# Kernel optimization log

Hardware: AMD Instinct MI355X
Metric: run time of the kernel (lower is better)

## Reference

```python
import jax, jax.numpy as jnp
import numpy as np
from jax import lax

IMG = 224.0
IOU_THRESH = 0.5

def box_cxcywh_to_xyxy(b):
    cx, cy, w, h = b[..., 0], b[..., 1], b[..., 2], b[..., 3]
    return jnp.stack([cx - 0.5 * w, cy - 0.5 * h, cx + 0.5 * w, cy + 0.5 * h], axis=-1)

def box_iou(a, b):
    area_a = (a[:, 2] - a[:, 0]) * (a[:, 3] - a[:, 1])
    area_b = (b[:, 2] - b[:, 0]) * (b[:, 3] - b[:, 1])
    lt = jnp.maximum(a[:, None, :2], b[None, :, :2])
    rb = jnp.minimum(a[:, None, 2:], b[None, :, 2:])
    wh = jnp.clip(rb - lt, 0.0)
    inter = wh[..., 0] * wh[..., 1]
    return inter / (area_a[:, None] + area_b[None, :] - inter)

def gumbel_softmax(key, logits, axis, tau=1.0):
    # straight-through hard gumbel-softmax (matches torch hard=True)
    g = jax.random.gumbel(key, logits.shape, logits.dtype)
    y = jax.nn.softmax((logits + g) / tau, axis=axis)
    y_hard = jax.nn.one_hot(jnp.argmax(y, axis=axis), y.shape[axis], axis=axis, dtype=y.dtype)
    return y + lax.stop_gradient(y_hard - y)

def nms_indices(boxes, scores, thresh):
    # iterative greedy NMS, returns kept indices in descending-score order (as torchvision)
    n = boxes.shape[0]
    order = jnp.argsort(-scores)
    b = boxes[order]
    areas = (b[:, 2] - b[:, 0]) * (b[:, 3] - b[:, 1])
    pos = jnp.arange(n)
    def body(i, suppressed):
        bi = b[i]
        lt = jnp.maximum(bi[:2], b[:, :2])
        rb = jnp.minimum(bi[2:], b[:, 2:])
        wh = jnp.clip(rb - lt, 0.0)
        inter = wh[:, 0] * wh[:, 1]
        iou = inter / (areas[i] + areas - inter)
        sup = (iou > thresh) & (pos > i) & jnp.logical_not(suppressed[i])
        return suppressed | sup
    suppressed = lax.fori_loop(0, n, body, jnp.zeros((n,), bool))
    keep = np.asarray(jnp.logical_not(suppressed))
    return jnp.asarray(np.asarray(order)[keep])

def _keys():
    return jax.random.split(jax.random.key(42), 3)

def _boxes_and_scores(classencodings, pred_logits, pred_boxes, tgt_ids, batch_idx, tgt_bbox, k0):
    C = classencodings.shape[0]
    B, Q, D = pred_logits.shape
    similarity = jnp.einsum('bqd,cd->bqc', pred_logits, classencodings)
    out_scores = jnp.max(similarity, axis=-1)
    clt = gumbel_softmax(k0, similarity, axis=-1)                      # [B,Q,C] hard
    offx = jnp.arange(C, dtype=pred_logits.dtype) * IMG
    offy = jnp.arange(B, dtype=pred_logits.dtype) * IMG
    ox = jnp.sum(clt * offx, axis=-1)                                  # [B,Q]
    oy = jnp.broadcast_to(offy[:, None], (B, Q))
    out_off = jnp.tile(jnp.stack([ox, oy], axis=-1), (1, 1, 2))        # [B,Q,4]
    out_bbox = (box_cxcywh_to_xyxy(pred_boxes) + out_off).reshape(-1, 4)
    f = pred_logits.dtype
    gt_off = jnp.tile(jnp.stack([IMG * tgt_ids.astype(f), IMG * batch_idx.astype(f)], axis=-1), (1, 2))
    tb = box_cxcywh_to_xyxy(tgt_bbox) + gt_off                         # [N,4]
    return similarity, out_scores.reshape(-1), out_bbox, tb

def ce_diag(logits):
    # CrossEntropyLoss(mean) with targets arange(n)
    return -jnp.mean(jnp.diagonal(jax.nn.log_softmax(logits, axis=1)))

def _forward(classencodings, pred_logits, pred_boxes, pred_masks, tgt_masks, tgt_embs, tgt_bbox, tgt_ids, batch_idx, nms_idx):
    k0, k1, k2 = _keys()
    B, Q, D = pred_logits.shape
    N = tgt_embs.shape[0]
    W, H = tgt_masks.shape[-2:]
    similarity, out_scores, out_bbox, tb = _boxes_and_scores(classencodings, pred_logits, pred_boxes, tgt_ids, batch_idx, tgt_bbox, k0)
    kept = out_bbox[nms_idx]                                           # [K,4]
    K = kept.shape[0]
    iou = box_iou(kept, tb)
    iou = jnp.where(jnp.isnan(iou), 0.0, iou)
    gt_log = jax.nn.softmax(iou, axis=1)
    gt_one_hot = gumbel_softmax(k1, gt_log, axis=1)                    # [K,N]
    gt_sel = gt_one_hot.T @ kept                                       # [N,4]
    gt_ious = jnp.diagonal(box_iou(gt_sel, tb))
    out_embs = gt_one_hot.T @ pred_logits.reshape(-1, D)[nms_idx]      # [N,D]
    class_loss = ce_diag(tgt_embs @ out_embs.T) + ce_diag(out_embs @ tgt_embs.T)
    scores = jnp.einsum('bqd,nd->bqn', pred_logits, tgt_embs).reshape(B * Q, N)
    ind = gumbel_softmax(k2, scores, axis=0).T                         # [N,B*Q]
    om = (ind @ pred_masks.reshape(B * Q, -1)).reshape(N, W, H)
    overall_mask_loss = jnp.mean((om - tgt_masks) ** 2)
    ocm = jnp.einsum('qwh,bcq->bcwh', om, similarity) / om.shape[1]    # [B,Q,W,H] (N==C==Q)
    ocm = jax.nn.softmax(ocm, axis=1)
    batch_lookup = jax.nn.one_hot(batch_idx, B, dtype=pred_logits.dtype).T  # [B,N]
    gt_sim = tgt_embs @ classencodings.T                               # [N,C]
    tsim = batch_lookup[:, :, None] * gt_sim[None, :, :]               # [B,N,C]
    gt_cm = jnp.einsum('bnc,nwh->bcwh', tsim, tgt_masks)               # [B,C,W,H]
    inp = ocm.reshape(B, -1)
    tgt = gt_cm.reshape(B, -1)
    dice = jnp.mean(jnp.sum(inp * tgt) / (jnp.sum(inp, -1) + jnp.sum(tgt, -1) + 1e-6))
    l1 = jnp.abs(gt_sel - tb).sum()
    return jnp.stack([class_loss, dice, overall_mask_loss / K, (1.0 - gt_ious).sum() / K, l1 / K])

def setup_inputs():
    key = jax.random.key(0)
    ks = jax.random.split(key, 10)
    B, Q, C, N, D, W, H = 8, 300, 300, 300, 256, 96, 96
    return {
        'classencodings': jax.random.normal(ks[0], (C, D), jnp.float32),
        'pred_logits': jax.random.normal(ks[1], (B, Q, D), jnp.float32),
        'pred_boxes': jax.random.uniform(ks[2], (B, Q, 4), jnp.float32),
        'pred_masks': jax.random.normal(ks[3], (B * Q, W, H), jnp.float32),
        'tgt_masks': jax.random.uniform(ks[4], (N, W, H), jnp.float32),
        'tgt_embs': jax.random.normal(ks[5], (N, D), jnp.float32),
        'tgt_bbox': jax.random.uniform(ks[6], (N, 4), jnp.float32),
        'im_masks': jnp.ones((B, 224, 224), jnp.float32),
        'tgt_ids': jax.random.randint(ks[7], (N,), 0, C, jnp.int32),
        'batch_idx': jnp.sort(jax.random.randint(ks[8], (N,), 0, B, jnp.int32)),
    }

def reference(classencodings, pred_logits, pred_boxes, pred_masks, tgt_masks, tgt_embs, tgt_bbox, im_masks, tgt_ids, batch_idx):
    k0, _, _ = _keys()
    _, scores, out_bbox, _ = _boxes_and_scores(classencodings, pred_logits, pred_boxes, tgt_ids, batch_idx, tgt_bbox, k0)
    nms_idx = nms_indices(out_bbox, scores, IOU_THRESH)
    return _forward(classencodings, pred_logits, pred_boxes, pred_masks, tgt_masks, tgt_embs, tgt_bbox, tgt_ids, batch_idx, nms_idx)
```

## Files before the change

### kernel.cpp

```cpp
#include <hip/hip_runtime.h>
#include <stdint.h>

#define DEVFN __device__ __forceinline__

typedef unsigned short u16;
typedef short bf16x8 __attribute__((ext_vector_type(8)));
typedef float f32x4 __attribute__((ext_vector_type(4)));

constexpr int BB = 8, QQ = 300, CC = 300, NN = 300, DD = 256;
constexpr int WHX = 9216, BQ = 2400, SIMW = 600;
constexpr int QP = 320;
constexpr int CP = 304;
constexpr int KP = 96;
constexpr int NP = 416;
constexpr int CELLCAP = 300;

constexpr size_t F_SIMS   = 0;
constexpr size_t F_GTSIM  = F_SIMS   + (size_t)BQ*SIMW;
constexpr size_t F_MM     = F_GTSIM  + (size_t)NN*CC;
constexpr size_t F_SCORE  = F_MM     + (size_t)NN*NN;
constexpr size_t F_BBOX   = F_SCORE  + BQ;
constexpr size_t F_TB     = F_BBOX   + (size_t)BQ*4;
constexpr size_t F_SB     = F_TB     + (size_t)NN*4;
constexpr size_t F_SAREA  = F_SB     + (size_t)BQ*4;
constexpr size_t F_KB     = F_SAREA  + BQ;
constexpr size_t F_ROWSUM = F_KB     + (size_t)BQ*4;
constexpr size_t F_OE     = F_ROWSUM + NN;
constexpr size_t F_GSEL   = F_OE     + (size_t)NN*DD;
constexpr size_t F_MSUM   = F_GSEL   + (size_t)NN*4;
constexpr size_t F_STGT   = F_MSUM   + NN;
constexpr size_t F_SC     = F_STGT   + 8;
constexpr size_t F_CNT    = F_SC     + 16;
constexpr size_t F_ACCEND = F_CNT    + BQ;
constexpr size_t F_ORDER  = F_ACCEND;
constexpr size_t F_NMSIDX = F_ORDER  + BQ;
constexpr size_t F_SEL2   = F_NMSIDX + BQ;
constexpr size_t F_BSTART = F_SEL2   + NN;
constexpr size_t F_KINT   = F_BSTART + 16;
constexpr size_t F_CLS    = F_KINT   + 4;
constexpr size_t F_KEEPF  = F_CLS    + BQ;
constexpr size_t F_LIST   = F_KEEPF  + BQ;
constexpr size_t F_S2T    = F_LIST   + (size_t)BQ*CELLCAP;
constexpr size_t F_SIMTB  = ((F_S2T + (size_t)NN*BQ + 7) & ~(size_t)7);
constexpr size_t F_OMT    = F_SIMTB + (size_t)BB*CP*QP/2;
constexpr size_t F_TMT    = F_OMT   + (size_t)WHX*QP/2;
constexpr size_t F_GTP    = F_TMT   + (size_t)WHX*NP/2;
constexpr size_t F_TOTAL  = F_GTP   + (size_t)BB*CP*KP/2;

DEVFN uint32_t rotl32(uint32_t v, int r){ return (v << r) | (v >> (32 - r)); }

DEVFN void tf2x32(uint32_t k0, uint32_t k1, uint32_t x0, uint32_t x1,
                  uint32_t& o0, uint32_t& o1){
  uint32_t ks2 = k0 ^ k1 ^ 0x1BD11BDAu;
  x0 += k0; x1 += k1;
#define TFR(r) x0 += x1; x1 = rotl32(x1, r); x1 ^= x0;
  TFR(13) TFR(15) TFR(26) TFR(6)   x0 += k1;  x1 += ks2 + 1u;
  TFR(17) TFR(29) TFR(16) TFR(24)  x0 += ks2; x1 += k0  + 2u;
  TFR(13) TFR(15) TFR(26) TFR(6)   x0 += k0;  x1 += k1  + 3u;
  TFR(17) TFR(29) TFR(16) TFR(24)  x0 += k1;  x1 += ks2 + 4u;
  TFR(13) TFR(15) TFR(26) TFR(6)   x0 += ks2; x1 += k0  + 5u;
#undef TFR
  o0 = x0; o1 = x1;
}

DEVFN void subkey(int i, uint32_t& k0, uint32_t& k1){
  tf2x32(0u, 42u, 0u, (uint32_t)i, k0, k1);
}

DEVFN float gumbel32(uint32_t k0, uint32_t k1, uint32_t idx){
  uint32_t h, l; tf2x32(k0, k1, 0u, idx, h, l);
  uint32_t bits = h ^ l;
  float f = __uint_as_float((bits >> 9) | 0x3F800000u) - 1.0f;
  const float tiny = 1.17549435e-38f;
  float u = fmaxf(tiny, f + tiny);
  return -logf(-logf(u));
}

DEVFN float iou_xyxy(float ax1,float ay1,float ax2,float ay2,
                     float bx1,float by1,float bx2,float by2){
  float aa = (ax2-ax1)*(ay2-ay1);
  float ab = (bx2-bx1)*(by2-by1);
  float lx = fmaxf(ax1,bx1), ly = fmaxf(ay1,by1);
  float rx = fminf(ax2,bx2), ry = fminf(ay2,by2);
  float iw = fmaxf(rx-lx,0.f), ih = fmaxf(ry-ly,0.f);
  float in_ = iw*ih;
  return in_/(aa+ab-in_);
}

DEVFN u16 f2bf(float x){
  uint32_t u = __float_as_uint(x);
  uint32_t r = u + 0x7FFFu + ((u >> 16) & 1u);
  return (u16)(r >> 16);
}

DEVFN void gload_lds16(const u16* g, u16* l){
  __builtin_amdgcn_global_load_lds(
      (const __attribute__((address_space(1))) unsigned int*)g,
      (__attribute__((address_space(3))) unsigned int*)l,
      16, 0, 0);
}

__global__ __launch_bounds__(256) void k_gemm_t(
    const float* __restrict__ pl, const float* __restrict__ ce,
    const float* __restrict__ te, float* __restrict__ sims,
    float* __restrict__ gtsim, float* __restrict__ s2t){
  __shared__ float As[16][64];
  __shared__ float Bs[16][64];
  const int row0 = blockIdx.x * 64, col0 = blockIdx.y * 64;
  const int tid = threadIdx.x;
  const int lrow = tid >> 2, lk0 = (tid & 3) * 4;
  const int tr = tid >> 4, tc = tid & 15;

  float acc[4][4];
  #pragma unroll
  for (int i = 0; i < 4; i++)
    #pragma unroll
    for (int j = 0; j < 4; j++) acc[i][j] = 0.f;

  const float4 z4 = {0.f,0.f,0.f,0.f};
  const int grow = row0 + lrow;
  const int gcol = col0 + lrow;
  const float* arow = nullptr;
  if (grow < 2400) arow = pl + (size_t)grow * DD;
  else if (grow < 2700) arow = te + (size_t)(grow - 2400) * DD;
  const float* brow = nullptr;
  if (gcol < 300) brow = ce + (size_t)gcol * DD;
  else if (gcol < 600) brow = te + (size_t)(gcol - 300) * DD;

  float4 av = arow ? *(const float4*)(arow + lk0) : z4;
  float4 bv = brow ? *(const float4*)(brow + lk0) : z4;

  for (int step = 0; step < 16; step++){
    __syncthreads();
    #pragma unroll
    for (int j = 0; j < 4; j++){
      As[lk0 + j][lrow] = ((const float*)&av)[j];
      Bs[lk0 + j][lrow] = ((const float*)&bv)[j];
    }
    __syncthreads();
    if (step + 1 < 16){
      const int k0 = (step + 1) * 16;
      av = arow ? *(const float4*)(arow + k0 + lk0) : z4;
      bv = brow ? *(const float4*)(brow + k0 + lk0) : z4;
    }
    #pragma unroll
    for (int kk = 0; kk < 16; kk++){
      float4 a4 = *(const float4*)&As[kk][tr*4];
      float4 b4 = *(const float4*)&Bs[kk][tc*4];
      float a[4] = {a4.x,a4.y,a4.z,a4.w};
      float b[4] = {b4.x,b4.y,b4.z,b4.w};
      #pragma unroll
      for (int i = 0; i < 4; i++)
        #pragma unroll
        for (int j = 0; j < 4; j++)
          acc[i][j] = fmaf(a[i], b[j], acc[i][j]);
    }
  }

  #pragma unroll
  for (int i = 0; i < 4; i++){
    const int r = row0 + tr*4 + i;
    const int c0 = col0 + tc*4;
    if (r < 2400){
      if (c0 < 600){
        float4 o0 = {acc[i][0],acc[i][1],acc[i][2],acc[i][3]};
        *(float4*)(sims + (size_t)r*SIMW + c0) = o0;
        if (c0 >= 300){
          #pragma unroll
          for (int j = 0; j < 4; j++)
            s2t[(size_t)(c0 + j - 300)*BQ + r] = acc[i][j];
        }
      }
    } else if (r < 2700){
      const int n = r - 2400;
      #pragma unroll
      for (int j = 0; j < 4; j++){
        int c = c0 + j;
        if (c < 300) gtsim[(size_t)n*CC + c] = acc[i][j];
      }
    }
  }
}

__global__ __launch_bounds__(64) void k_post(
    const float* __restrict__ sims, const float* __restrict__ pb,
    const float* __restrict__ tbb, const int* __restrict__ tids,
    const int* __restrict__ bidx, const float* __restrict__ gtsim,
    float* __restrict__ score, float* __restrict__ bbox,
    float* __restrict__ tb, float* __restrict__ rowsum,
    int* __restrict__ clsout){
  const int bq = blockIdx.x;
  const int lane = threadIdx.x;
  float v[5];
  #pragma unroll
  for (int k = 0; k < 5; k++){
    int c = lane + 64*k;
    v[k] = (c < CC) ? sims[(size_t)bq*SIMW + c] : -INFINITY;
  }
  float mx = v[0];
  #pragma unroll
  for (int k = 1; k < 5; k++) mx = fmaxf(mx, v[k]);
  #pragma unroll
  for (int o = 1; o < 64; o <<= 1) mx = fmaxf(mx, __shfl_xor(mx, o));
  if (lane == 0) score[bq] = mx;

  uint32_t gk0, gk1; subkey(0, gk0, gk1);
  float besty = -INFINITY; int besti = 0x7fffffff;
  #pragma unroll
  for (int k = 0; k < 5; k++){
    int c = lane + 64*k;
    if (c < CC){
      float y = v[k] + gumbel32(gk0, gk1, (uint32_t)(bq*CC + c));
      if (y > besty || (y == besty && c < besti)){ besty = y; besti = c; }
    }
  }
  #pragma unroll
  for (int o = 1; o < 64; o <<= 1){
    float oy = __shfl_xor(besty, o);
    int   oi = __shfl_xor(besti, o);
    if (oy > besty || (oy == besty && oi < besti)){ besty = oy; besti = oi; }
  }
  if (lane == 0){
    int cls = besti;
    clsout[bq] = cls;
    float ox = 224.0f * (float)cls;
    float oy2 = 224.0f * (float)(bq / QQ);
    float cx = pb[bq*4+0], cy = pb[bq*4+1], ww = pb[bq*4+2], hh = pb[bq*4+3];
    bbox[bq*4+0] = cx - 0.5f*ww + ox;
    bbox[bq*4+1] = cy - 0.5f*hh + oy2;
    bbox[bq*4+2] = cx + 0.5f*ww + ox;
    bbox[bq*4+3] = cy + 0.5f*hh + oy2;
  }
  if (bq < NN){
    float rs = 0.f;
    #pragma unroll
    for (int k = 0; k < 5; k++){
      int c = lane + 64*k;
      if (c < CC) rs += gtsim[(size_t)bq*CC + c];
    }
    #pragma unroll
    for (int o = 1; o < 64; o <<= 1) rs += __shfl_xor(rs, o);
    if (lane == 0) rowsum[bq] = rs;
    if (lane == 1){
      float gx = 224.0f * (float)tids[bq], gy = 224.0f * (float)bidx[bq];
      float cx = tbb[bq*4+0], cy = tbb[bq*4+1], ww = tbb[bq*4+2], hh = tbb[bq*4+3];
      tb[bq*4+0] = cx - 0.5f*ww + gx;
      tb[bq*4+1] = cy - 0.5f*hh + gy;
      tb[bq*4+2] = cx + 0.5f*ww + gx;
      tb[bq*4+3] = cy + 0.5f*hh + gy;
    }
  }
}

__global__ __launch_bounds__(256) void k_rankgather(
    const float* __restrict__ score, const float* __restrict__ bbox,
    const int* __restrict__ cls, const int* __restrict__ bidx,
    int* __restrict__ order, float* __restrict__ sb,
    int* __restrict__ bstart, int* __restrict__ cnt,
    int* __restrict__ list){
  const int t = blockIdx.x;
  const int tid = threadIdx.x;
  const float st = score[t];
  int c = 0;
  for (int j = tid; j < BQ; j += 256){
    float sj = score[j];
    c += (sj > st) || (sj == st && j < t);
  }
  #pragma unroll
  for (int o = 1; o < 64; o <<= 1) c += __shfl_xor(c, o);
  __shared__ int wsum[4];
  if ((tid & 63) == 0) wsum[tid >> 6] = c;
  __syncthreads();
  if (tid == 0){
    int r = wsum[0] + wsum[1] + wsum[2] + wsum[3];
    order[r] = t;
    float x1 = bbox[t*4+0], y1 = bbox[t*4+1], x2 = bbox[t*4+2], y2 = bbox[t*4+3];
    sb[r*4+0] = x1; sb[r*4+1] = y1; sb[r*4+2] = x2; sb[r*4+3] = y2;
    int key = (t / QQ) * CC + cls[t];
    int slot = atomicAdd(&cnt[key], 1);
    list[(size_t)key*CELLCAP + slot] = r;
  }
  if (t == 0 && tid >= 32 && tid < 41){
    int b = tid - 32, cb = 0;
    for (int n = 0; n < NN; n++) cb += (bidx[n] < b);
    bstart[b] = cb;
  }
}

__global__ __launch_bounds__(256) void k_cellnms(
    const float* __restrict__ sb, const int* __restrict__ cnt,
    const int* __restrict__ list, int* __restrict__ keepf){
  int key = blockIdx.x*256 + threadIdx.x;
  if (key >= BB*CC) return;
  int m = cnt[key];
  if (m <= 0) return;
  const int* lst = list + (size_t)key*CELLCAP;
  unsigned long long keptmask = 0ull;
  int prevp = -1;
  for (int a = 0; a < m; a++){
    int pa = 0x7fffffff;
    for (int j = 0; j < m; j++){
      int pj = lst[j];
      if (pj > prevp && pj < pa) pa = pj;
    }
    prevp = pa;
    float4 A = ((const float4*)sb)[pa];
    float areaA = (A.z-A.x)*(A.w-A.y);
    bool kept = true;
    int pbprev = -1;
    for (int b2 = 0; b2 < a; b2++){
      int pb = 0x7fffffff;
      for (int j = 0; j < m; j++){
        int pj = lst[j];
        if (pj > pbprev && pj < pb) pb = pj;
      }
      pbprev = pb;
      bool keptb = (m <= 64) ? (((keptmask >> b2) & 1ull) != 0ull) : (keepf[pb] != 0);
      if (!keptb) continue;
      float4 B = ((const float4*)sb)[pb];
      float areaB = (B.z-B.x)*(B.w-B.y);
      float lx = fmaxf(A.x,B.x), ly = fmaxf(A.y,B.y);
      float rx = fminf(A.z,B.z), ry = fminf(A.w,B.w);
      float iw = fmaxf(rx-lx,0.f), ih = fmaxf(ry-ly,0.f);
      float inter = iw*ih;
      if (inter/(areaA + areaB - inter) > 0.5f){ kept = false; break; }
    }
    if (m <= 64 && kept) keptmask |= (1ull << a);
    keepf[pa] = kept ? 1 : 0;
  }
}

__global__ __launch_bounds__(256) void k_compact(
    const int* __restrict__ keepflag, const int* __restrict__ order,
    const float* __restrict__ sb, int* __restrict__ nmsidx,
    float* __restrict__ kb, int* __restrict__ kint){
  __shared__ int csum[256];
  int tid = threadIdx.x;
  int p0 = tid*10;
  int keepf[10];
  int cnt = 0;
  #pragma unroll
  for (int d = 0; d < 10; d++){
    int p = p0 + d;
    int k = 0;
    if (p < BQ) k = keepflag[p];
    keepf[d] = k; cnt += k;
  }
  csum[tid] = cnt; __syncthreads();
  for (int s = 1; s < 256; s <<= 1){
    int add = (tid >= s) ? csum[tid - s] : 0;
    __syncthreads();
    csum[tid] += add;
    __syncthreads();
  }
  int pos = csum[tid] - cnt;
  #pragma unroll
  for (int d = 0; d < 10; d++){
    if (keepf[d]){
      int p = p0 + d;
      nmsidx[pos] = order[p];
      ((float4*)kb)[pos] = ((const float4*)sb)[p];
      pos++;
    }
  }
  if (tid == 255) kint[0] = csum[255];
}

__global__ __launch_bounds__(64) void k_gtsel(
    const float* __restrict__ kb, const float* __restrict__ tb,
    const int* __restrict__ nmsidx, const float* __restrict__ pl,
    const int* __restrict__ kint, float* __restrict__ gsel,
    float* __restrict__ oe){
  const int k = blockIdx.x;
  if (k >= kint[0]) return;
  const int lane = threadIdx.x;
  float4 a = ((const float4*)kb)[k];
  float iou[5];
  float mx = -INFINITY;
  #pragma unroll
  for (int j = 0; j < 5; j++){
    int n = lane + 64*j;
    if (n < NN){
      float4 t = ((const float4*)tb)[n];
      float u = iou_xyxy(a.x,a.y,a.z,a.w, t.x,t.y,t.z,t.w);
      if (u != u) u = 0.f;
      iou[j] = u;
      mx = fmaxf(mx, u);
    } else iou[j] = -INFINITY;
  }
  #pragma unroll
  for (int o = 1; o < 64; o <<= 1) mx = fmaxf(mx, __shfl_xor(mx, o));
  float e[5];
  float ssum = 0.f;
  #pragma unroll
  for (int j = 0; j < 5; j++){
    int n = lane + 64*j;
    e[j] = (n < NN) ? expf(iou[j] - mx) : 0.f;
    ssum += e[j];
  }
  #pragma unroll
  for (int o = 1; o < 64; o <<= 1) ssum += __shfl_xor(ssum, o);
  uint32_t gk0, gk1; subkey(1, gk0, gk1);
  float besty = -INFINITY; int besti = 0x7fffffff;
  #pragma unroll
  for (int j = 0; j < 5; j++){
    int n = lane + 64*j;
    if (n < NN){
      float y = e[j] / ssum + gumbel32(gk0, gk1, (uint32_t)(k*NN + n));
      if (y > besty || (y == besty && n < besti)){ besty = y; besti = n; }
    }
  }
  #pragma unroll
  for (int o = 1; o < 64; o <<= 1){
    float oy = __shfl_xor(besty, o);
    int   oi = __shfl_xor(besti, o);
    if (oy > besty || (oy == besty && oi < besti)){ besty = oy; besti = oi; }
  }
  const int sel = besti;
  if (lane < 4) atomicAdd(&gsel[sel*4 + lane], ((const float*)&a)[lane]);
  const float* plrow = pl + (size_t)nmsidx[k]*DD;
  #pragma unroll
  for (int j = 0; j < 4; j++){
    int c = lane + 64*j;
    atomicAdd(&oe[(size_t)sel*DD + c], plrow[c]);
  }
}

__global__ __launch_bounds__(256) void k_m_t(
    const float* __restrict__ te, const float* __restrict__ oe,
    float* __restrict__ M){
  __shared__ float As[16][32];
  __shared__ float Bs[16][32];
  const int row0 = blockIdx.x * 32, col0 = blockIdx.y * 32;
  const int tid = threadIdx.x;
  const int lr = tid >> 3, lk0 = (tid & 7) * 2;
  const int tr = tid >> 4, tc = tid & 15;
  float acc[2][2] = {{0.f,0.f},{0.f,0.f}};
  const float* arow = (row0 + lr < NN) ? te + (size_t)(row0 + lr)*DD : nullptr;
  const float* brow = (col0 + lr < NN) ? oe + (size_t)(col0 + lr)*DD : nullptr;
  for (int step = 0; step < 16; step++){
    const int k0 = step*16;
    float2 a2 = arow ? *(const float2*)(arow + k0 + lk0) : float2{0.f,0.f};
    float2 b2 = brow ? *(const float2*)(brow + k0 + lk0) : float2{0.f,0.f};
    __syncthreads();
    As[lk0][lr] = a2.x; As[lk0+1][lr] = a2.y;
    Bs[lk0][lr] = b2.x; Bs[lk0+1][lr] = b2.y;
    __syncthreads();
    #pragma unroll
    for (int kk = 0; kk < 16; kk++){
      float a0 = As[kk][tr*2], a1 = As[kk][tr*2+1];
      float b0 = Bs[kk][tc*2], b1 = Bs[kk][tc*2+1];
      acc[0][0] = fmaf(a0,b0,acc[0][0]);
      acc[0][1] = fmaf(a0,b1,acc[0][1]);
      acc[1][0] = fmaf(a1,b0,acc[1][0]);
      acc[1][1] = fmaf(a1,b1,acc[1][1]);
    }
  }
  #pragma unroll
  for (int i = 0; i < 2; i++){
    int r = row0 + tr*2 + i;
    if (r >= NN) continue;
    #pragma unroll
    for (int j = 0; j < 2; j++){
      int c = col0 + tc*2 + j;
      if (c < NN) M[(size_t)r*NN + c] = acc[i][j];
    }
  }
}

__global__ __launch_bounds__(64) void k_ce(
    const float* __restrict__ M, float* __restrict__ sc){
  int i = blockIdx.x, lane = threadIdx.x;
  float m = -INFINITY;
  for (int j = lane; j < NN; j += 64) m = fmaxf(m, M[(size_t)i*NN + j]);
  for (int o = 32; o > 0; o >>= 1) m = fmaxf(m, __shfl_xor(m, o));
  float s = 0.f;
  for (int j = lane; j < NN; j += 64) s += expf(M[(size_t)i*NN + j] - m);
  for (int o = 32; o > 0; o >>= 1) s += __shfl_xor(s, o);
  float lr = m + logf(s);
  float m2 = -INFINITY;
  for (int j = lane; j < NN; j += 64) m2 = fmaxf(m2, M[(size_t)j*NN + i]);
  for (int o = 32; o > 0; o >>= 1) m2 = fmaxf(m2, __shfl_xor(m2, o));
  float s2 = 0.f;
  for (int j = lane; j < NN; j += 64) s2 += expf(M[(size_t)j*NN + i] - m2);
  for (int o = 32; o > 0; o >>= 1) s2 += __shfl_xor(s2, o);
  float lc = m2 + logf(s2);
  if (lane == 0){
    float d = M[(size_t)i*NN + i];
    atomicAdd(&sc[0], lr - d);
    atomicAdd(&sc[1], lc - d);
  }
}

__global__ __launch_bounds__(256) void k_sel2(
    const float* __restrict__ s2t, int* __restrict__ sel2){
  int n = blockIdx.x, tid = threadIdx.x;
  uint32_t gk0, gk1; subkey(2, gk0, gk1);
  float best = -INFINITY; int bi = 0x7fffffff;
  for (int r = tid; r < BQ; r += 256){
    float v = s2t[(size_t)n*BQ + r] + gumbel32(gk0, gk1, (uint32_t)(r*NN + n));
    if (v > best){ best = v; bi = r; }
  }
  __shared__ float sv[256];
  __shared__ int   si[256];
  sv[tid] = best; si[tid] = bi; __syncthreads();
  for (int s = 128; s > 0; s >>= 1){
    if (tid < s){
      float ov = sv[tid+s]; int oi = si[tid+s];
      if (ov > sv[tid] || (ov == sv[tid] && oi < si[tid])){ sv[tid] = ov; si[tid] = oi; }
    }
    __syncthreads();
  }
  if (tid == 0) sel2[n] = si[0];
}

constexpr int PB_SIMT = 400;
constexpr int PB_OMT  = 1440;
constexpr int PB_TMT  = 1872;
constexpr int PB_GTP  = 114;
__global__ __launch_bounds__(256) void k_pack(
    const float* __restrict__ sims, const float* __restrict__ pm,
    const float* __restrict__ tm, const float* __restrict__ gtsim,
    const int* __restrict__ sel2, const int* __restrict__ bstart,
    u16* __restrict__ simTb, u16* __restrict__ omT,
    u16* __restrict__ tmT, u16* __restrict__ gtp,
    float* __restrict__ msum, float* __restrict__ sc){
  __shared__ float ld[32][65];
  __shared__ float sm_ts[32];
  __shared__ float sm_d2;
  const int blk = blockIdx.x;
  const int tid = threadIdx.x;

  if (blk < PB_SIMT){
    int bx = blk % 10, by = (blk / 10) % 5, b = blk / 50;
    int q0 = bx*32, c0 = by*64;
    for (int i = tid; i < 32*64; i += 256){
      int qi = i >> 6, ci = i & 63;
      int q = q0 + qi, c = c0 + ci;
      ld[qi][ci] = (q < QQ && c < CC) ? sims[((size_t)b*QQ + q)*SIMW + c] : 0.f;
    }
    __syncthreads();
    int cloc = tid >> 2, j0 = (tid & 3)*8;
    int c = c0 + cloc;
    if (c < CP){
      u16 tmp[8];
      #pragma unroll
      for (int j = 0; j < 8; j++) tmp[j] = f2bf(ld[j0+j][cloc]);
      *(uint4*)(simTb + ((size_t)b*CP + c)*QP + q0 + j0) = *(const uint4*)tmp;
    }
  } else if (blk < PB_SIMT + PB_OMT){
    int r = blk - PB_SIMT;
    int q0 = (r % 10)*32, wh0 = (r / 10)*64;
    if (tid < 32) sm_ts[tid] = 0.f;
    if (tid == 32) sm_d2 = 0.f;
    __syncthreads();
    float d2loc = 0.f;
    for (int i = tid; i < 32*64; i += 256){
      int qi = i >> 6, wi = i & 63;
      int q = q0 + qi;
      float pv = 0.f;
      if (q < QQ){
        pv = pm[(size_t)sel2[q]*WHX + wh0 + wi];
        float tv = tm[(size_t)q*WHX + wh0 + wi];
        float d = pv - tv;
        d2loc += d*d;
        atomicAdd(&sm_ts[qi], tv);
      }
      ld[qi][wi] = pv;
    }
    atomicAdd(&sm_d2, d2loc);
    __syncthreads();
    int wloc = tid >> 2, j0 = (tid & 3)*8;
    u16 tmp[8];
    #pragma unroll
    for (int j = 0; j < 8; j++) tmp[j] = f2bf(ld[j0+j][wloc] * (1.0f/96.0f));
    *(uint4*)(omT + (size_t)(wh0+wloc)*QP + q0 + j0) = *(const uint4*)tmp;
    if (tid < 32 && q0 + tid < NN) atomicAdd(&msum[q0 + tid], sm_ts[tid]);
    if (tid == 32) atomicAdd(&sc[2], sm_d2);
  } else if (blk < PB_SIMT + PB_OMT + PB_TMT){
    int r = blk - PB_SIMT - PB_OMT;
    int n0 = (r % 13)*32, wh0 = (r / 13)*64;
    for (int i = tid; i < 32*64; i += 256){
      int ni = i >> 6, wi = i & 63;
      int n = n0 + ni;
      ld[ni][wi] = (n < NN) ? tm[(size_t)n*WHX + wh0 + wi] : 0.f;
    }
    __syncthreads();
    int wloc = tid >> 2, j0 = (tid & 3)*8;
    u16 tmp[8];
    #pragma unroll
    for (int j = 0; j < 8; j++) tmp[j] = f2bf(ld[j0+j][wloc]);
    *(uint4*)(tmT + (size_t)(wh0+wloc)*NP + n0 + j0) = *(const uint4*)tmp;
  } else {
    int g = (blk - PB_SIMT - PB_OMT - PB_TMT)*256 + tid;
    int b = g / (CP*(KP/8));
    int rem = g - b*(CP*(KP/8));
    int c = rem / (KP/8);
    int kg = rem % (KP/8);
    int n0 = bstart[b], n1 = bstart[b+1];
    int kst = n0 & ~7;
    u16 tmp[8];
    #pragma unroll
    for (int j = 0; j < 8; j++){
      int n = kst + kg*8 + j;
      float v = (n >= n0 && n < n1 && c < CC) ? gtsim[(size_t)n*CC + c] : 0.f;
      tmp[j] = f2bf(v);
    }
    *(uint4*)(gtp + ((size_t)b*CP + c)*KP + kg*8) = *(const uint4*)tmp;
  }
}

constexpr int ALDS = 32;
__global__ __launch_bounds__(256) void k_zsoft(
    const u16* __restrict__ simTb, const u16* __restrict__ omT,
    const u16* __restrict__ gtp, const u16* __restrict__ tmT,
    const int* __restrict__ bstart, float* __restrict__ sc){
  const int bid = blockIdx.x;
  const int xcd = bid & 7;
  const int r9  = bid >> 3;
  const int tile = xcd * 18 + (r9 % 18);
  const int b    = r9 / 18;
  const int tid = threadIdx.x;
  const int w = tid >> 6, l = tid & 63;
  const int lrow = l & 15, lgrp = l >> 4;
  const int col = tile*64 + w*16 + lrow;

  __shared__ u16 As[2][CP*ALDS];
  __shared__ float red[256];

  const u16* Ab = simTb + (size_t)b*CP*QP;
  int srcoff[5];
  #pragma unroll
  for (int i = 0; i < 5; i++){
    int p = (w*5 + i)*64 + l;
    int row = p >> 2, cs = p & 3;
    int g = cs ^ ((row >> 1) & 3);
    srcoff[i] = row*QP + g*8;
  }
  const int nIss = (w == 3) ? 4 : 5;
  const int roff = (lgrp ^ ((lrow >> 1) & 3)) << 3;
  const u16* pB = omT + (size_t)col*QP + lgrp*8;

  #pragma unroll
  for (int i = 0; i < 5; i++){
    if (i < nIss) gload_lds16(Ab + srcoff[i], &As[0][(w*5+i)*512]);
  }
  bf16x8 bcur = *(const bf16x8*)(pB);

  f32x4 acc[19];
  #pragma unroll
  for (int t = 0; t < 19; t++) acc[t] = (f32x4){0.f,0.f,0.f,0.f};
  __syncthreads();

  for (int ks = 0; ks < 10; ks++){
    const int cur = ks & 1;
    bf16x8 bnext;
    if (ks + 1 < 10){
      const int ko = (ks + 1) * 32;
      #pragma unroll
      for (int i = 0; i < 5; i++){
        if (i < nIss) gload_lds16(Ab + srcoff[i] + ko, &As[cur ^ 1][(w*5+i)*512]);
      }
      bnext = *(const bf16x8*)(pB + ko);
    }
    __builtin_amdgcn_s_setprio(1);
    #pragma unroll
    for (int t = 0; t < 19; t++){
      bf16x8 af = *(const bf16x8*)&As[cur][t*16*ALDS + lrow*ALDS + roff];
      acc[t] = __builtin_amdgcn_mfma_f32_16x16x32_bf16(af, bcur, acc[t], 0, 0, 0);
    }
    __builtin_amdgcn_s_setprio(0);
    bcur = bnext;
    __syncthreads();
  }

  float lmax = -INFINITY;
  #pragma unroll
  for (int t = 0; t < 19; t++){
    if (t == 18 && lgrp == 3) continue;
    lmax = fmaxf(lmax, fmaxf(fmaxf(acc[t][0], acc[t][1]), fmaxf(acc[t][2], acc[t][3])));
  }
  lmax = fmaxf(lmax, __shfl_xor(lmax, 16));
  lmax = fmaxf(lmax, __shfl_xor(lmax, 32));
  float ls = 0.f;
  #pragma unroll
  for (int t = 0; t < 19; t++){
    if (t == 18 && lgrp == 3){
      acc[t] = (f32x4){0.f,0.f,0.f,0.f};
      continue;
    }
    float p0 = __expf(acc[t][0] - lmax);
    float p1 = __expf(acc[t][1] - lmax);
    float p2 = __expf(acc[t][2] - lmax);
    float p3 = __expf(acc[t][3] - lmax);
    acc[t][0] = p0; acc[t][1] = p1; acc[t][2] = p2; acc[t][3] = p3;
    ls += p0 + p1 + p2 + p3;
  }
  float S = ls;
  S += __shfl_xor(S, 16);
  S += __shfl_xor(S, 32);
  float inv = 1.f / S;

  const int n0 = bstart[b];
  const int kst = n0 & ~7;
  const u16* tB = tmT + (size_t)col*NP + kst + lgrp*8;
  bf16x8 b2a = *(const bf16x8*)(tB);
  bf16x8 b2b = *(const bf16x8*)(tB + 32);
  bf16x8 b2c = *(const bf16x8*)(tB + 64);
  const u16* A2 = gtp + (size_t)b*CP*KP + (size_t)lrow*KP + lgrp*8;
  float dl = 0.f;
  #pragma unroll
  for (int t = 0; t < 19; t++){
    const u16* ar = A2 + (size_t)t*16*KP;
    f32x4 rr = (f32x4){0.f,0.f,0.f,0.f};
    rr = __builtin_amdgcn_mfma_f32_16x16x32_bf16(*(const bf16x8*)(ar),      b2a, rr, 0, 0, 0);
    rr = __builtin_amdgcn_mfma_f32_16x16x32_bf16(*(const bf16x8*)(ar + 32), b2b, rr, 0, 0, 0);
    rr = __builtin_amdgcn_mfma_f32_16x16x32_bf16(*(const bf16x8*)(ar + 64), b2c, rr, 0, 0, 0);
    dl += acc[t][0]*rr[0] + acc[t][1]*rr[1] + acc[t][2]*rr[2] + acc[t][3]*rr[3];
  }
  dl *= inv;

  red[tid] = dl; __syncthreads();
  for (int s = 128; s > 0; s >>= 1){
    if (tid < s) red[tid] += red[tid+s];
    __syncthreads();
  }
  if (tid == 0) atomicAdd(&sc[5], red[0]);
}

__global__ __launch_bounds__(512) void k_final3(
    const float* __restrict__ gsel, const float* __restrict__ tb,
    const int* __restrict__ bidx, const float* __restrict__ rowsum,
    const float* __restrict__ msum, const float* __restrict__ sc,
    const int* __restrict__ kint, float* __restrict__ out){
  int tid = threadIdx.x;
  __shared__ float s1[512], s2[512];
  __shared__ float stgt[8];
  if (tid < 8) stgt[tid] = 0.f;
  __syncthreads();
  float a1 = 0.f, a2 = 0.f;
  if (tid < NN){
    float4 g = ((const float4*)gsel)[tid];
    float4 t = ((const float4*)tb)[tid];
    float iou = iou_xyxy(g.x,g.y,g.z,g.w, t.x,t.y,t.z,t.w);
    a1 = 1.f - iou;
    a2 = fabsf(g.x-t.x) + fabsf(g.y-t.y) + fabsf(g.z-t.z) + fabsf(g.w-t.w);
    atomicAdd(&stgt[bidx[tid]], rowsum[tid] * msum[tid]);
  }
  s1[tid] = a1; s2[tid] = a2; __syncthreads();
  for (int s = 256; s > 0; s >>= 1){
    if (tid < s){ s1[tid] += s1[tid+s]; s2[tid] += s2[tid+s]; }
    __syncthreads();
  }
  if (tid == 0){
    float K = (float)kint[0];
    float cls = sc[0]/300.f + sc[1]/300.f;
    float stot = sc[5];
    float dice = 0.f;
    for (int b = 0; b < 8; b++) dice += stot / (9216.0f + stgt[b] + 1e-6f);
    dice *= (1.0f/8.0f);
    out[0] = cls;
    out[1] = dice;
    out[2] = (sc[2] / 2764800.0f) / K;
    out[3] = s1[0] / K;
    out[4] = s2[0] / K;
  }
}

extern "C" void kernel_launch(void* const* d_in, const int* in_sizes, int n_in,
                              void* d_out, int out_size, void* d_ws, size_t ws_size,
                              hipStream_t stream) {
  const float* ce  = (const float*)d_in[0];
  const float* pl  = (const float*)d_in[1];
  const float* pb  = (const float*)d_in[2];
  const float* pm  = (const float*)d_in[3];
  const float* tm  = (const float*)d_in[4];
  const float* te  = (const float*)d_in[5];
  const float* tbb = (const float*)d_in[6];
  const int*  tids = (const int*)d_in[8];
  const int*  bidx = (const int*)d_in[9];
  float* out = (float*)d_out;
  float* w = (float*)d_ws;

  if (ws_size < F_TOTAL * sizeof(float)) return;

  float* SIMS   = w + F_SIMS;
  float* GTSIM  = w + F_GTSIM;
  float* MM     = w + F_MM;
  float* SCORE  = w + F_SCORE;
  float* BBOX   = w + F_BBOX;
  float* TBOX   = w + F_TB;
  float* SB     = w + F_SB;
  float* KB     = w + F_KB;
  float* ROWSUM = w + F_ROWSUM;
  float* OE     = w + F_OE;
  float* GSEL   = w + F_GSEL;
  float* MSUM   = w + F_MSUM;
  float* SC     = w + F_SC;
  float* S2T    = w + F_S2T;
  int*   CNT    = (int*)(w + F_CNT);
  int*   ORDER  = (int*)(w + F_ORDER);
  int*   NMSIDX = (int*)(w + F_NMSIDX);
  int*   SEL2   = (int*)(w + F_SEL2);
  int*   BSTART = (int*)(w + F_BSTART);
  int*   KINT   = (int*)(w + F_KINT);
  int*   CLS    = (int*)(w + F_CLS);
  int*   KEEPF  = (int*)(w + F_KEEPF);
  int*   LIST   = (int*)(w + F_LIST);
  u16* SIMTB = (u16*)(w + F_SIMTB);
  u16* OMT   = (u16*)(w + F_OMT);
  u16* TMT   = (u16*)(w + F_TMT);
  u16* GTP   = (u16*)(w + F_GTP);

  hipMemsetAsync(w + F_OE, 0, (F_ACCEND - F_OE) * sizeof(float), stream);

  k_gemm_t<<<dim3(43, 10), 256, 0, stream>>>(pl, ce, te, SIMS, GTSIM, S2T);
  k_post<<<BQ, 64, 0, stream>>>(SIMS, pb, tbb, tids, bidx, GTSIM, SCORE, BBOX, TBOX, ROWSUM, CLS);
  k_rankgather<<<BQ, 256, 0, stream>>>(SCORE, BBOX, CLS, bidx, ORDER, SB, BSTART, CNT, LIST);
  k_sel2<<<NN, 256, 0, stream>>>(S2T, SEL2);
  k_pack<<<PB_SIMT + PB_OMT + PB_TMT + PB_GTP, 256, 0, stream>>>(
      SIMS, pm, tm, GTSIM, SEL2, BSTART, SIMTB, OMT, TMT, GTP, MSUM, SC);
  k_cellnms<<<(BB*CC + 255)/256, 256, 0, stream>>>(SB, CNT, LIST, KEEPF);
  k_compact<<<1, 256, 0, stream>>>(KEEPF, ORDER, SB, NMSIDX, KB, KINT);
  k_gtsel<<<BQ, 64, 0, stream>>>(KB, TBOX, NMSIDX, pl, KINT, GSEL, OE);
  k_m_t<<<dim3(10, 10), 256, 0, stream>>>(te, OE, MM);
  k_ce<<<NN, 64, 0, stream>>>(MM, SC);
  k_zsoft<<<dim3((WHX/64) * BB), 256, 0, stream>>>(SIMTB, OMT, GTP, TMT, BSTART, SC);
  k_final3<<<1, 512, 0, stream>>>(GSEL, TBOX, bidx, ROWSUM, MSUM, SC, KINT, out);
}
```

Before: 233.0 us.

## Fuse cell NMS with compaction, merge mask pack passes, shuffle-reduce in zsoft

Per-cell NMS and the keep-flag compaction now run in one single-block kernel, with keep flags held in shared memory, so one launch and a global round-trip go away. In k_pack, the pred-mask and target-mask transpose blocks are merged so each target mask tile is read once and feeds both the tmT and omT outputs. The final reduction in k_zsoft changes from a shared-memory tree to wavefront shuffles plus a 4-entry shared array. The cost is that cell NMS now runs over 2400 cells with only 256 threads in one block, where it previously spread across about 10 blocks, so that stage gets less parallelism.

```diff
diff --git a/kernel.cpp b/kernel.cpp
--- a/kernel.cpp
+++ b/kernel.cpp
@@ -287,73 +287,73 @@
   }
 }
 
-__global__ __launch_bounds__(256) void k_cellnms(
+__global__ __launch_bounds__(256) void k_cellcompact(
     const float* __restrict__ sb, const int* __restrict__ cnt,
-    const int* __restrict__ list, int* __restrict__ keepf){
-  int key = blockIdx.x*256 + threadIdx.x;
-  if (key >= BB*CC) return;
-  int m = cnt[key];
-  if (m <= 0) return;
-  const int* lst = list + (size_t)key*CELLCAP;
-  unsigned long long keptmask = 0ull;
-  int prevp = -1;
-  for (int a = 0; a < m; a++){
-    int pa = 0x7fffffff;
-    for (int j = 0; j < m; j++){
-      int pj = lst[j];
-      if (pj > prevp && pj < pa) pa = pj;
-    }
-    prevp = pa;
-    float4 A = ((const float4*)sb)[pa];
-    float areaA = (A.z-A.x)*(A.w-A.y);
-    bool kept = true;
-    int pbprev = -1;
-    for (int b2 = 0; b2 < a; b2++){
-      int pb = 0x7fffffff;
+    const int* __restrict__ list, const int* __restrict__ order,
+    int* __restrict__ nmsidx, float* __restrict__ kb, int* __restrict__ kint){
+  __shared__ int keepfL[BQ];
+  __shared__ int csum[256];
+  const int tid = threadIdx.x;
+  for (int p = tid; p < BQ; p += 256) keepfL[p] = 0;
+  __syncthreads();
+
+  for (int key = tid; key < BB*CC; key += 256){
+    int m = cnt[key];
+    if (m <= 0) continue;
+    const int* lst = list + (size_t)key*CELLCAP;
+    unsigned long long keptmask = 0ull;
+    int prevp = -1;
+    for (int a = 0; a < m; a++){
+      int pa = 0x7fffffff;
       for (int j = 0; j < m; j++){
         int pj = lst[j];
-        if (pj > pbprev && pj < pb) pb = pj;
+        if (pj > prevp && pj < pa) pa = pj;
       }
-      pbprev = pb;
-      bool keptb = (m <= 64) ? (((keptmask >> b2) & 1ull) != 0ull) : (keepf[pb] != 0);
-      if (!keptb) continue;
-      float4 B = ((const float4*)sb)[pb];
-      float areaB = (B.z-B.x)*(B.w-B.y);
-      float lx = fmaxf(A.x,B.x), ly = fmaxf(A.y,B.y);
-      float rx = fminf(A.z,B.z), ry = fminf(A.w,B.w);
-      float iw = fmaxf(rx-lx,0.f), ih = fmaxf(ry-ly,0.f);
-      float inter = iw*ih;
-      if (inter/(areaA + areaB - inter) > 0.5f){ kept = false; break; }
-    }
-    if (m <= 64 && kept) keptmask |= (1ull << a);
-    keepf[pa] = kept ? 1 : 0;
-  }
-}
-
-__global__ __launch_bounds__(256) void k_compact(
-    const int* __restrict__ keepflag, const int* __restrict__ order,
-    const float* __restrict__ sb, int* __restrict__ nmsidx,
-    float* __restrict__ kb, int* __restrict__ kint){
-  __shared__ int csum[256];
-  int tid = threadIdx.x;
+      prevp = pa;
+      float4 A = ((const float4*)sb)[pa];
+      float areaA = (A.z-A.x)*(A.w-A.y);
+      bool kept = true;
+      int pbprev = -1;
+      for (int b2 = 0; b2 < a; b2++){
+        int pb = 0x7fffffff;
+        for (int j = 0; j < m; j++){
+          int pj = lst[j];
+          if (pj > pbprev && pj < pb) pb = pj;
+        }
+        pbprev = pb;
+        bool keptb = (m <= 64) ? (((keptmask >> b2) & 1ull) != 0ull) : (keepfL[pb] != 0);
+        if (!keptb) continue;
+        float4 B = ((const float4*)sb)[pb];
+        float areaB = (B.z-B.x)*(B.w-B.y);
+        float lx = fmaxf(A.x,B.x), ly = fmaxf(A.y,B.y);
+        float rx = fminf(A.z,B.z), ry = fminf(A.w,B.w);
+        float iw = fmaxf(rx-lx,0.f), ih = fmaxf(ry-ly,0.f);
+        float inter = iw*ih;
+        if (inter/(areaA + areaB - inter) > 0.5f){ kept = false; break; }
+      }
+      if (m <= 64 && kept) keptmask |= (1ull << a);
+      keepfL[pa] = kept ? 1 : 0;
+    }
+  }
+  __syncthreads();
+
   int p0 = tid*10;
   int keepf[10];
-  int cnt = 0;
+  int cntk = 0;
   #pragma unroll
   for (int d = 0; d < 10; d++){
     int p = p0 + d;
-    int k = 0;
-    if (p < BQ) k = keepflag[p];
-    keepf[d] = k; cnt += k;
-  }
-  csum[tid] = cnt; __syncthreads();
+    int k = (p < BQ) ? keepfL[p] : 0;
+    keepf[d] = k; cntk += k;
+  }
+  csum[tid] = cntk; __syncthreads();
   for (int s = 1; s < 256; s <<= 1){
     int add = (tid >= s) ? csum[tid - s] : 0;
     __syncthreads();
     csum[tid] += add;
     __syncthreads();
   }
-  int pos = csum[tid] - cnt;
+  int pos = csum[tid] - cntk;
   #pragma unroll
   for (int d = 0; d < 10; d++){
     if (keepf[d]){
@@ -515,8 +515,7 @@
 }
 
 constexpr int PB_SIMT = 400;
-constexpr int PB_OMT  = 1440;
-constexpr int PB_TMT  = 1872;
+constexpr int PB_OMTM = 1872;
 constexpr int PB_GTP  = 114;
 __global__ __launch_bounds__(256) void k_pack(
     const float* __restrict__ sims, const float* __restrict__ pm,
@@ -525,7 +524,8 @@
     u16* __restrict__ simTb, u16* __restrict__ omT,
     u16* __restrict__ tmT, u16* __restrict__ gtp,
     float* __restrict__ msum, float* __restrict__ sc){
-  __shared__ float ld[32][65];
+  __shared__ float ldP[32][65];
+  __shared__ float ldT[32][65];
   __shared__ float sm_ts[32];
   __shared__ float sm_d2;
   const int blk = blockIdx.x;
@@ -537,7 +537,7 @@
     for (int i = tid; i < 32*64; i += 256){
       int qi = i >> 6, ci = i & 63;
       int q = q0 + qi, c = c0 + ci;
-      ld[qi][ci] = (q < QQ && c < CC) ? sims[((size_t)b*QQ + q)*SIMW + c] : 0.f;
+      ldP[qi][ci] = (q < QQ && c < CC) ? sims[((size_t)b*QQ + q)*SIMW + c] : 0.f;
     }
     __syncthreads();
     int cloc = tid >> 2, j0 = (tid & 3)*8;
@@ -545,12 +545,15 @@
     if (c < CP){
       u16 tmp[8];
       #pragma unroll
-      for (int j = 0; j < 8; j++) tmp[j] = f2bf(ld[j0+j][cloc]);
+      for (int j = 0; j < 8; j++) tmp[j] = f2bf(ldP[j0+j][cloc]);
       *(uint4*)(simTb + ((size_t)b*CP + c)*QP + q0 + j0) = *(const uint4*)tmp;
     }
-  } else if (blk < PB_SIMT + PB_OMT){
+  } else if (blk < PB_SIMT + PB_OMTM){
     int r = blk - PB_SIMT;
-    int q0 = (r % 10)*32, wh0 = (r / 10)*64;
+    int qt = r % 13;
+    int wh0 = (r / 13) * 64;
+    int q0 = qt * 32;
+    const bool doOm = (qt < 10);
     if (tid < 32) sm_ts[tid] = 0.f;
     if (tid == 32) sm_d2 = 0.f;
     __syncthreads();
@@ -558,41 +561,38 @@
     for (int i = tid; i < 32*64; i += 256){
       int qi = i >> 6, wi = i & 63;
       int q = q0 + qi;
-      float pv = 0.f;
-      if (q < QQ){
-        pv = pm[(size_t)sel2[q]*WHX + wh0 + wi];
-        float tv = tm[(size_t)q*WHX + wh0 + wi];
-        float d = pv - tv;
-        d2loc += d*d;
-        atomicAdd(&sm_ts[qi], tv);
+      float tv = (q < NN) ? tm[(size_t)q*WHX + wh0 + wi] : 0.f;
+      ldT[qi][wi] = tv;
+      if (doOm){
+        float pv = 0.f;
+        if (q < QQ){
+          pv = pm[(size_t)sel2[q]*WHX + wh0 + wi];
+          float d = pv - tv;
+          d2loc += d*d;
+          atomicAdd(&sm_ts[qi], tv);
+        }
+        ldP[qi][wi] = pv;
       }
-      ld[qi][wi] = pv;
-    }
-    atomicAdd(&sm_d2, d2loc);
+    }
+    if (doOm) atomicAdd(&sm_d2, d2loc);
     __syncthreads();
     int wloc = tid >> 2, j0 = (tid & 3)*8;
-    u16 tmp[8];
-    #pragma unroll
-    for (int j = 0; j < 8; j++) tmp[j] = f2bf(ld[j0+j][wloc] * (1.0f/96.0f));
-    *(uint4*)(omT + (size_t)(wh0+wloc)*QP + q0 + j0) = *(const uint4*)tmp;
-    if (tid < 32 && q0 + tid < NN) atomicAdd(&msum[q0 + tid], sm_ts[tid]);
-    if (tid == 32) atomicAdd(&sc[2], sm_d2);
-  } else if (blk < PB_SIMT + PB_OMT + PB_TMT){
-    int r = blk - PB_SIMT - PB_OMT;
-    int n0 = (r % 13)*32, wh0 = (r / 13)*64;
-    for (int i = tid; i < 32*64; i += 256){
-      int ni = i >> 6, wi = i & 63;
-      int n = n0 + ni;
-      ld[ni][wi] = (n < NN) ? tm[(size_t)n*WHX + wh0 + wi] : 0.f;
-    }
-    __syncthreads();
-    int wloc = tid >> 2, j0 = (tid & 3)*8;
-    u16 tmp[8];
-    #pragma unroll
-    for (int j = 0; j < 8; j++) tmp[j] = f2bf(ld[j0+j][wloc]);
-    *(uint4*)(tmT + (size_t)(wh0+wloc)*NP + n0 + j0) = *(const uint4*)tmp;
+    {
+      u16 tmp[8];
+      #pragma unroll
+      for (int j = 0; j < 8; j++) tmp[j] = f2bf(ldT[j0+j][wloc]);
+      *(uint4*)(tmT + (size_t)(wh0+wloc)*NP + q0 + j0) = *(const uint4*)tmp;
+    }
+    if (doOm){
+      u16 tmp[8];
+      #pragma unroll
+      for (int j = 0; j < 8; j++) tmp[j] = f2bf(ldP[j0+j][wloc] * (1.0f/96.0f));
+      *(uint4*)(omT + (size_t)(wh0+wloc)*QP + q0 + j0) = *(const uint4*)tmp;
+      if (tid < 32 && q0 + tid < NN) atomicAdd(&msum[q0 + tid], sm_ts[tid]);
+      if (tid == 32) atomicAdd(&sc[2], sm_d2);
+    }
   } else {
-    int g = (blk - PB_SIMT - PB_OMT - PB_TMT)*256 + tid;
+    int g = (blk - PB_SIMT - PB_OMTM)*256 + tid;
     int b = g / (CP*(KP/8));
     int rem = g - b*(CP*(KP/8));
     int c = rem / (KP/8);
@@ -626,7 +626,7 @@
   const int col = tile*64 + w*16 + lrow;
 
   __shared__ u16 As[2][CP*ALDS];
-  __shared__ float red[256];
+  __shared__ float red[4];
 
   const u16* Ab = simTb + (size_t)b*CP*QP;
   int srcoff[5];
@@ -720,12 +720,11 @@
   }
   dl *= inv;
 
-  red[tid] = dl; __syncthreads();
-  for (int s = 128; s > 0; s >>= 1){
-    if (tid < s) red[tid] += red[tid+s];
-    __syncthreads();
-  }
-  if (tid == 0) atomicAdd(&sc[5], red[0]);
+  #pragma unroll
+  for (int o = 1; o < 64; o <<= 1) dl += __shfl_xor(dl, o);
+  if (l == 0) red[w] = dl;
+  __syncthreads();
+  if (tid == 0) atomicAdd(&sc[5], red[0] + red[1] + red[2] + red[3]);
 }
 
 __global__ __launch_bounds__(512) void k_final3(
@@ -805,7 +804,6 @@
   int*   BSTART = (int*)(w + F_BSTART);
   int*   KINT   = (int*)(w + F_KINT);
   int*   CLS    = (int*)(w + F_CLS);
-  int*   KEEPF  = (int*)(w + F_KEEPF);
   int*   LIST   = (int*)(w + F_LIST);
   u16* SIMTB = (u16*)(w + F_SIMTB);
   u16* OMT   = (u16*)(w + F_OMT);
@@ -818,10 +816,9 @@
   k_post<<<BQ, 64, 0, stream>>>(SIMS, pb, tbb, tids, bidx, GTSIM, SCORE, BBOX, TBOX, ROWSUM, CLS);
   k_rankgather<<<BQ, 256, 0, stream>>>(SCORE, BBOX, CLS, bidx, ORDER, SB, BSTART, CNT, LIST);
   k_sel2<<<NN, 256, 0, stream>>>(S2T, SEL2);
-  k_pack<<<PB_SIMT + PB_OMT + PB_TMT + PB_GTP, 256, 0, stream>>>(
+  k_pack<<<PB_SIMT + PB_OMTM + PB_GTP, 256, 0, stream>>>(
       SIMS, pm, tm, GTSIM, SEL2, BSTART, SIMTB, OMT, TMT, GTP, MSUM, SC);
-  k_cellnms<<<(BB*CC + 255)/256, 256, 0, stream>>>(SB, CNT, LIST, KEEPF);
-  k_compact<<<1, 256, 0, stream>>>(KEEPF, ORDER, SB, NMSIDX, KB, KINT);
+  k_cellcompact<<<1, 256, 0, stream>>>(SB, CNT, LIST, ORDER, NMSIDX, KB, KINT);
   k_gtsel<<<BQ, 64, 0, stream>>>(KB, TBOX, NMSIDX, pl, KINT, GSEL, OE);
   k_m_t<<<dim3(10, 10), 256, 0, stream>>>(te, OE, MM);
   k_ce<<<NN, 64, 0, stream>>>(MM, SC);
```

Result: slower. 325.8 us (+39.9%).
